# Kernel optimization log

Hardware: AMD Instinct MI355X
Metric: run time of the kernel (lower is better)

## Reference

```python
import jax, jax.numpy as jnp
import numpy as np

B, L, H = 32, 512, 256


def _gru(x, h, Wih, Whh, bih, bhh):
    # torch.nn.GRUCell math: gates ordered [r, z, n]
    gi = x @ Wih.T + bih
    gh = h @ Whh.T + bhh
    ir, iz, inn = jnp.split(gi, 3, axis=-1)
    hr, hz, hn = jnp.split(gh, 3, axis=-1)
    r = jax.nn.sigmoid(ir + hr)
    z = jax.nn.sigmoid(iz + hz)
    n = jnp.tanh(inn + r * hn)
    return (1.0 - z) * n + z * h


def setup_inputs() -> dict:
    key = jax.random.key(0)
    ks = jax.random.split(key, 20)
    s = 1.0 / np.sqrt(H)
    u = lambda k, shape: jax.random.uniform(k, shape, jnp.float32, -s, s)
    return {
        "P": jax.random.normal(ks[0], (B, L, H), jnp.float32),
        "wq_w": u(ks[1], (H, H)), "wq_b": u(ks[2], (H,)),
        "wp_w": u(ks[3], (H, H)), "wp_b": u(ks[4], (H,)),
        "ws_w": u(ks[5], (1, H)), "ws_b": u(ks[6], (1,)),
        "wg_w": u(ks[7], (H, 2 * H)), "wg_b": u(ks[8], (H,)),
        "Wih_l": u(ks[9], (3 * H, H)), "Whh_l": u(ks[10], (3 * H, H)),
        "bih_l": u(ks[11], (3 * H,)), "bhh_l": u(ks[12], (3 * H,)),
        "Wih_r": u(ks[13], (3 * H, H)), "Whh_r": u(ks[14], (3 * H, H)),
        "bih_r": u(ks[15], (3 * H,)), "bhh_r": u(ks[16], (3 * H,)),
    }


def reference(P, wq_w, wq_b, wp_w, wp_b, ws_w, ws_b, wg_w, wg_b,
              Wih_l, Whh_l, bih_l, bhh_l, Wih_r, Whh_r, bih_r, bhh_r):
    b, l, h = P.shape
    # wq(P) and wp(P[:,i]) are recomputed identically each step in the
    # original; hoist them once (same math).
    Hq = P @ wq_w.T + wq_b          # [B,L,H]
    Pp = P @ wp_w.T + wp_b          # [B,L,H]

    def left_step(hc, xs):
        p, pq = xs                  # [B,H], [B,H]
        # scores_j = ws . tanh(wq(P_j) + wp(p))
        scores = jnp.einsum('blh,h->bl', jnp.tanh(Hq + pq[:, None, :]), ws_w[0]) + ws_b[0]
        attn = jax.nn.softmax(scores, axis=1)
        c = jnp.einsum('bl,blh->bh', attn, P)
        g = jax.nn.sigmoid(jnp.concatenate([p, c], axis=1) @ wg_w.T + wg_b)
        c = g * c
        h_new = _gru(c, hc, Wih_l, Whh_l, bih_l, bhh_l)
        return h_new, (h_new, c)

    h0 = jnp.zeros((b, h), P.dtype)
    Pt = jnp.transpose(P, (1, 0, 2))   # [L,B,H]
    Ppt = jnp.transpose(Pp, (1, 0, 2))
    _, (out_l, c_seq) = jax.lax.scan(left_step, h0, (Pt, Ppt))

    def right_step(hc, c):
        h_new = _gru(c, hc, Wih_r, Whh_r, bih_r, bhh_r)
        return h_new, h_new

    _, out_r_rev = jax.lax.scan(right_step, h0, c_seq[::-1])
    out_r = out_r_rev[::-1]

    out = jnp.concatenate([out_l, out_r], axis=2)  # [L,B,2H]
    return jnp.transpose(out, (1, 0, 2))           # [B,L,2H]
```

## Files before the change

kernel.cpp:

```cpp
#include <hip/hip_runtime.h>
#include <cstdint>


#define LL 512
#define HH 256

typedef _Float16 half2_t __attribute__((ext_vector_type(2)));
typedef _Float16 f16x8   __attribute__((ext_vector_type(8)));
typedef float    f32x4   __attribute__((ext_vector_type(4)));

__device__ __forceinline__ float exp2f_fast(float x){
#if defined(__HIP_DEVICE_COMPILE__)
  return __builtin_amdgcn_exp2f(x);
#else
  return exp2f(x);
#endif
}
__device__ __forceinline__ float rcpf_fast(float x){
#if defined(__HIP_DEVICE_COMPILE__)
  return __builtin_amdgcn_rcpf(x);
#else
  return 1.0f/x;
#endif
}
__device__ __forceinline__ float tanh_fast(float x){
  float e = exp2f_fast(x * 2.885390081777927f);
  return 1.0f - 2.0f * rcpf_fast(1.0f + e);
}
__device__ __forceinline__ float sigmoid_fast(float x){
  return rcpf_fast(1.0f + exp2f_fast(x * -1.4426950408889634f));
}

#define SCALE_K2 2.885390081777927f

#if defined(__HIP_DEVICE_COMPILE__) && __has_builtin(__builtin_amdgcn_fdot2)
#define USE_FDOT2 1
#endif

__device__ __forceinline__ float dot2_acc(unsigned wb, unsigned hb, float a){
  half2_t wv = __builtin_bit_cast(half2_t, wb);
  half2_t hv = __builtin_bit_cast(half2_t, hb);
#ifdef USE_FDOT2
  return __builtin_amdgcn_fdot2(wv, hv, a, false);
#else
  return a + (float)wv.x*(float)hv.x + (float)wv.y*(float)hv.y;
#endif
}

__device__ __forceinline__ unsigned pack2h(float a, float b){
  half2_t h = { (_Float16)a, (_Float16)b };
  return __builtin_bit_cast(unsigned, h);
}

__device__ __forceinline__ void stage_t128(float* Ls, const float* g, int ldg){
  int tid = threadIdx.x;
  int r = tid >> 4, kq = (tid & 15) * 4;
  #pragma unroll
  for (int it = 0; it < 8; it++){
    int rr = r + 16*it;
    float4 v = *(const float4*)(g + (size_t)rr*ldg + kq);
    Ls[(kq+0)*132 + rr] = v.x;
    Ls[(kq+1)*132 + rr] = v.y;
    Ls[(kq+2)*132 + rr] = v.z;
    Ls[(kq+3)*132 + rr] = v.w;
  }
}
__device__ __forceinline__ void rg_inner128(const float* Xs, const float* Ws,
                                            float (&acc)[8][8], int rg, int cg){
  #pragma unroll 2
  for (int k = 0; k < 64; k++){
    const float* xr = Xs + k*132;
    const float* wr = Ws + k*132;
    float4 x0 = *(const float4*)(xr + rg*4);
    float4 x1 = *(const float4*)(xr + 64 + rg*4);
    float4 w0 = *(const float4*)(wr + cg*4);
    float4 w1 = *(const float4*)(wr + 64 + cg*4);
    float xv[8] = {x0.x,x0.y,x0.z,x0.w, x1.x,x1.y,x1.z,x1.w};
    float wv[8] = {w0.x,w0.y,w0.z,w0.w, w1.x,w1.y,w1.z,w1.w};
    #pragma unroll
    for (int i=0;i<8;i++)
      #pragma unroll
      for (int j=0;j<8;j++)
        acc[i][j] = fmaf(xv[i], wv[j], acc[i][j]);
  }
}
#define ROW_OF(i, rg) ((rg)*4 + ((i)&3) + ((i)>>2)*64)
#define COL_OF(j, cg) ((cg)*4 + ((j)&3) + ((j)>>2)*64)

#define LDK 36

__device__ __forceinline__ void mstage_direct(unsigned* Ls, const float* g, int ldg){
  int tid = threadIdx.x;
  int row = tid >> 1, half = tid & 1;
  const float4* s = (const float4*)(g + (size_t)row*ldg + half*32);
  unsigned* d = Ls + row*LDK + half*16;
  #pragma unroll
  for (int i = 0; i < 8; i += 2){
    float4 a = s[i], b = s[i+1];
    uint4 o;
    o.x = pack2h(a.x,a.y); o.y = pack2h(a.z,a.w);
    o.z = pack2h(b.x,b.y); o.w = pack2h(b.z,b.w);
    *(uint4*)(d + i*2) = o;
  }
}
__device__ __forceinline__ void mstage_trans(unsigned* Ls, const float* g, int ldg){
  int tid = threadIdx.x;
  int j = (tid & 31) * 4, kq = tid >> 5;
  #pragma unroll
  for (int it = 0; it < 4; it++){
    int kp = kq*4 + it;
    float4 a = *(const float4*)(g + (size_t)(2*kp  )*ldg + j);
    float4 b = *(const float4*)(g + (size_t)(2*kp+1)*ldg + j);
    Ls[(j+0)*LDK + kp] = pack2h(a.x, b.x);
    Ls[(j+1)*LDK + kp] = pack2h(a.y, b.y);
    Ls[(j+2)*LDK + kp] = pack2h(a.z, b.z);
    Ls[(j+3)*LDK + kp] = pack2h(a.w, b.w);
  }
}
__device__ __forceinline__ void mfma_inner(const unsigned* As, const unsigned* Bs,
                                           f32x4 (&acc)[8][2], int w, int l){
  int lr = l & 15, lq = l >> 4;
  #pragma unroll
  for (int kt = 0; kt < 2; kt++){
    f16x8 bf0, bf1;
    {
      uint4 q0 = *(const uint4*)&Bs[(w*32 +      lr)*LDK + kt*16 + lq*4];
      uint4 q1 = *(const uint4*)&Bs[(w*32 + 16 + lr)*LDK + kt*16 + lq*4];
      bf0 = __builtin_bit_cast(f16x8, q0);
      bf1 = __builtin_bit_cast(f16x8, q1);
    }
    #pragma unroll
    for (int rf = 0; rf < 8; rf++){
      uint4 qa = *(const uint4*)&As[(rf*16 + lr)*LDK + kt*16 + lq*4];
      f16x8 af = __builtin_bit_cast(f16x8, qa);
      acc[rf][0] = __builtin_amdgcn_mfma_f32_16x16x32_f16(af, bf0, acc[rf][0], 0,0,0);
      acc[rf][1] = __builtin_amdgcn_mfma_f32_16x16x32_f16(af, bf1, acc[rf][1], 0,0,0);
    }
  }
}

__global__ __launch_bounds__(256) void k1_hq_pp(
    const float* __restrict__ P,
    const float* __restrict__ wq_w, const float* __restrict__ wq_b,
    const float* __restrict__ wp_w, const float* __restrict__ wp_b,
    float* __restrict__ HQ, float* __restrict__ PP)
{
  __shared__ __align__(16) float Xs[64*132];
  __shared__ __align__(16) float Ws[64*132];
  int rt = blockIdx.x, ct = blockIdx.y;
  const float* W  = (ct < 2) ? wq_w : wp_w;
  const float* Bv = (ct < 2) ? wq_b : wp_b;
  float* O = (ct < 2) ? HQ : PP;
  int c0 = (ct & 1) * 128, r0 = rt * 128;
  int tid = threadIdx.x, rg = tid & 15, cg = tid >> 4;
  float acc[8][8];
  #pragma unroll
  for (int i=0;i<8;i++)
    #pragma unroll
    for (int j=0;j<8;j++) acc[i][j]=0.f;
  for (int kc = 0; kc < 4; kc++){
    __syncthreads();
    stage_t128(Xs, P + (size_t)r0*HH + kc*64, HH);
    stage_t128(Ws, W + (size_t)c0*HH + kc*64, HH);
    __syncthreads();
    rg_inner128(Xs, Ws, acc, rg, cg);
  }
  float bj[8];
  #pragma unroll
  for (int j=0;j<8;j++) bj[j] = Bv[c0 + COL_OF(j,cg)];
  #pragma unroll
  for (int i=0;i<8;i++){
    int r = r0 + ROW_OF(i,rg);
    #pragma unroll
    for (int j=0;j<8;j++)
      O[(size_t)r*HH + c0 + COL_OF(j,cg)] = SCALE_K2 * (acc[i][j] + bj[j]);
  }
}

__global__ __launch_bounds__(256) void k2_scores(
    const float* __restrict__ HQ, const float* __restrict__ PP,
    const float* __restrict__ ws_w, float* __restrict__ S)
{
  __shared__ float Hq_c[128*65];
  __shared__ float Pp_c[32*65];
  __shared__ float wsl[256];
  int tid = threadIdx.x;
  int b = blockIdx.y, t0 = blockIdx.x * 32;
  wsl[tid] = ws_w[tid];
  int tg = tid >> 6;
  int lg = tid & 63;
  for (int lc = 0; lc < 4; lc++){
    float acc[8][2];
    #pragma unroll
    for (int i=0;i<8;i++){ acc[i][0]=0.f; acc[i][1]=0.f; }
    for (int hc = 0; hc < 4; hc++){
      __syncthreads();
      {
        int r = tid >> 4, kq = (tid & 15) * 4;
        #pragma unroll
        for (int it=0; it<2; it++){
          int t = r + 16*it;
          float4 v = *(const float4*)(PP + ((size_t)b*LL + t0 + t)*HH + hc*64 + kq);
          float* d = Pp_c + t*65 + kq;
          d[0]=v.x; d[1]=v.y; d[2]=v.z; d[3]=v.w;
        }
      }
      {
        int r = tid >> 4, kq = (tid & 15) * 4;
        #pragma unroll
        for (int it=0; it<8; it++){
          int l = r + 16*it;
          float4 v = *(const float4*)(HQ + ((size_t)b*LL + lc*128 + l)*HH + hc*64 + kq);
          float* d = Hq_c + l*65 + kq;
          d[0]=v.x; d[1]=v.y; d[2]=v.z; d[3]=v.w;
        }
      }
      __syncthreads();
      #pragma unroll 2
      for (int h = 0; h < 64; h++){
        float w = wsl[hc*64 + h];
        float pp[8], hq[2];
        #pragma unroll
        for (int i=0;i<8;i++) pp[i] = Pp_c[(tg + 4*i)*65 + h];
        #pragma unroll
        for (int j=0;j<2;j++) hq[j] = Hq_c[(2*lg + j)*65 + h];
        #pragma unroll
        for (int i=0;i<8;i++)
          #pragma unroll
          for (int j=0;j<2;j++){
            float e = exp2f_fast(pp[i] + hq[j]);
            acc[i][j] = fmaf(w, rcpf_fast(1.0f + e), acc[i][j]);
          }
      }
    }
    #pragma unroll
    for (int i=0;i<8;i++)
      #pragma unroll
      for (int j=0;j<2;j++)
        S[((size_t)b*LL + t0 + tg + 4*i)*LL + lc*128 + 2*lg + j] = -2.0f*acc[i][j];
    __syncthreads();
  }
}

__global__ __launch_bounds__(256) void k3_softmax(float* __restrict__ S)
{
  int wave = threadIdx.x >> 6, lane = threadIdx.x & 63;
  size_t row = (size_t)blockIdx.x*4 + wave;
  float* p = S + row*LL;
  float v[8];
  #pragma unroll
  for (int i=0;i<8;i++) v[i] = p[lane + 64*i];
  float m = v[0];
  #pragma unroll
  for (int i=1;i<8;i++) m = fmaxf(m, v[i]);
  #pragma unroll
  for (int off=32; off>=1; off>>=1) m = fmaxf(m, __shfl_xor(m, off, 64));
  float s = 0.f;
  #pragma unroll
  for (int i=0;i<8;i++){ v[i] = exp2f_fast((v[i]-m)*1.4426950408889634f); s += v[i]; }
  #pragma unroll
  for (int off=32; off>=1; off>>=1) s += __shfl_xor(s, off, 64);
  float inv = 1.0f / s;
  #pragma unroll
  for (int i=0;i<8;i++) p[lane + 64*i] = v[i]*inv;
}

__global__ __launch_bounds__(256, 4) void k4_context(
    const float* __restrict__ S, const float* __restrict__ P, float* __restrict__ C)
{
  __shared__ __align__(16) unsigned As[128*LDK];
  __shared__ __align__(16) unsigned Bs[128*LDK];
  int j0 = blockIdx.x * 128, t0 = blockIdx.y * 128, b = blockIdx.z;
  int tid = threadIdx.x, w = tid >> 6, l = tid & 63;
  f32x4 acc[8][2];
  #pragma unroll
  for (int i=0;i<8;i++){ acc[i][0]=(f32x4){0,0,0,0}; acc[i][1]=(f32x4){0,0,0,0}; }
  for (int lc = 0; lc < 8; lc++){
    int l0 = lc*64;
    __syncthreads();
    mstage_direct(As, S + ((size_t)b*LL + t0)*LL + l0, LL);
    mstage_trans (Bs, P + ((size_t)b*LL + l0)*HH + j0, HH);
    __syncthreads();
    mfma_inner(As, Bs, acc, w, l);
  }
  int lr = l & 15, lq = l >> 4;
  #pragma unroll
  for (int rf=0; rf<8; rf++)
    #pragma unroll
    for (int cf=0; cf<2; cf++){
      int col = j0 + w*32 + cf*16 + lr;
      #pragma unroll
      for (int r=0; r<4; r++){
        int row = t0 + rf*16 + lq*4 + r;
        C[((size_t)b*LL + row)*HH + col] = acc[rf][cf][r];
      }
    }
}

__global__ __launch_bounds__(256, 4) void k5_gate(
    const float* __restrict__ P, const float* __restrict__ C,
    const float* __restrict__ wg_w, const float* __restrict__ wg_b,
    float* __restrict__ CG)
{
  __shared__ __align__(16) unsigned As[128*LDK];
  __shared__ __align__(16) unsigned Bs[128*LDK];
  int r0 = blockIdx.x*128, c0 = blockIdx.y*128;
  int tid = threadIdx.x, w = tid >> 6, l = tid & 63;
  f32x4 acc[8][2];
  #pragma unroll
  for (int i=0;i<8;i++){ acc[i][0]=(f32x4){0,0,0,0}; acc[i][1]=(f32x4){0,0,0,0}; }
  for (int kc = 0; kc < 8; kc++){
    const float* Xsrc = (kc < 4) ? (P + (size_t)r0*HH + kc*64)
                                 : (C + (size_t)r0*HH + (kc-4)*64);
    __syncthreads();
    mstage_direct(As, Xsrc, HH);
    mstage_direct(Bs, wg_w + (size_t)c0*(2*HH) + kc*64, 2*HH);
    __syncthreads();
    mfma_inner(As, Bs, acc, w, l);
  }
  int lr = l & 15, lq = l >> 4;
  #pragma unroll
  for (int cf=0; cf<2; cf++){
    int col = c0 + w*32 + cf*16 + lr;
    float bj = wg_b[col];
    #pragma unroll
    for (int rf=0; rf<8; rf++)
      #pragma unroll
      for (int r=0; r<4; r++){
        int row = r0 + rf*16 + lq*4 + r;
        float g = sigmoid_fast(acc[rf][cf][r] + bj);
        CG[(size_t)row*HH + col] = g * C[(size_t)row*HH + col];
      }
  }
}

__global__ __launch_bounds__(256, 4) void k6_gi(
    const float* __restrict__ CG,
    const float* __restrict__ Wih_l, const float* __restrict__ bih_l,
    const float* __restrict__ Wih_r, const float* __restrict__ bih_r,
    float* __restrict__ GIL, float* __restrict__ GIR)
{
  __shared__ __align__(16) unsigned As[128*LDK];
  __shared__ __align__(16) unsigned Bs[128*LDK];
  int rt = blockIdx.x, ct = blockIdx.y;
  int dir = (ct >= 6);
  const float* Wih = dir ? Wih_r : Wih_l;
  const float* bih = dir ? bih_r : bih_l;
  float* GI = dir ? GIR : GIL;
  int c0 = (ct % 6) * 128, r0 = rt * 128;
  int tid = threadIdx.x, w = tid >> 6, l = tid & 63;
  f32x4 acc[8][2];
  #pragma unroll
  for (int i=0;i<8;i++){ acc[i][0]=(f32x4){0,0,0,0}; acc[i][1]=(f32x4){0,0,0,0}; }
  for (int kc = 0; kc < 4; kc++){
    __syncthreads();
    mstage_direct(As, CG  + (size_t)r0*HH + kc*64, HH);
    mstage_direct(Bs, Wih + (size_t)c0*HH + kc*64, HH);
    __syncthreads();
    mfma_inner(As, Bs, acc, w, l);
  }
  int lr = l & 15, lq = l >> 4;
  #pragma unroll
  for (int cf=0; cf<2; cf++){
    int col = c0 + w*32 + cf*16 + lr;
    float bj = bih[col];
    #pragma unroll
    for (int rf=0; rf<8; rf++)
      #pragma unroll
      for (int r=0; r<4; r++){
        int row = r0 + rf*16 + lq*4 + r;
        GI[(size_t)row*768 + col] = acc[rf][cf][r] + bj;
      }
  }
}

__global__ __launch_bounds__(512, 2) void k7_scan(
    const float* __restrict__ GIL, const float* __restrict__ GIR,
    const float* __restrict__ Whh_l, const float* __restrict__ bhh_l,
    const float* __restrict__ Whh_r, const float* __restrict__ bhh_r,
    float* __restrict__ out)
{
  int b   = blockIdx.x >> 1;
  int dir = blockIdx.x & 1;
  int t   = threadIdx.x;
  int u   = t >> 1;
  int ks  = t & 1;
  int k0  = ks * 128;
  const float* GI  = dir ? GIR : GIL;
  const float* Whh = dir ? Whh_r : Whh_l;
  const float* bhh = dir ? bhh_r : bhh_l;

  unsigned w_r[64], w_z[64], w_n[64];
  {
    const float2* wr = (const float2*)(Whh + (size_t)(u      )*HH + k0);
    const float2* wz = (const float2*)(Whh + (size_t)(u + 256)*HH + k0);
    const float2* wn = (const float2*)(Whh + (size_t)(u + 512)*HH + k0);
    #pragma unroll
    for (int pc = 0; pc < 8; pc++){
      #pragma unroll
      for (int p = pc*8; p < pc*8+8; p++){ float2 a = wr[p]; w_r[p] = pack2h(a.x, a.y); }
      __builtin_amdgcn_sched_barrier(0);
      #pragma unroll
      for (int p = pc*8; p < pc*8+8; p++){ float2 a = wz[p]; w_z[p] = pack2h(a.x, a.y); }
      __builtin_amdgcn_sched_barrier(0);
      #pragma unroll
      for (int p = pc*8; p < pc*8+8; p++){ float2 a = wn[p]; w_n[p] = pack2h(a.x, a.y); }
      __builtin_amdgcn_sched_barrier(0);
    }
  }
  float b_r = bhh[u], b_z = bhh[u + 256], b_n = bhh[u + 512];

  __shared__ __align__(16) unsigned hsbuf[2][128];
  __shared__ __align__(16) float gi_buf[32*768];
  __shared__ __align__(16) float out_buf[32*256];
  if (t < 128){ hsbuf[0][t] = 0; }

  float hprev = 0.f;

  #pragma unroll 1
  for (int chunk = 0; chunk < 16; chunk++){
    int s0 = chunk * 32;
    int tlo = dir ? (LL - s0 - 32) : s0;
    {
      const float4* src = (const float4*)(GI + ((size_t)b*LL + tlo)*768);
      float4* dst = (float4*)gi_buf;
      #pragma unroll
      for (int rd = 0; rd < 3; rd++){
        float4 v0 = src[t + 512*(4*rd+0)];
        float4 v1 = src[t + 512*(4*rd+1)];
        float4 v2 = src[t + 512*(4*rd+2)];
        float4 v3 = src[t + 512*(4*rd+3)];
        dst[t + 512*(4*rd+0)] = v0;
        dst[t + 512*(4*rd+1)] = v1;
        dst[t + 512*(4*rd+2)] = v2;
        dst[t + 512*(4*rd+3)] = v3;
        __builtin_amdgcn_sched_barrier(0);
      }
    }
    __syncthreads();

    #pragma unroll 1
    for (int p = 0; p < 32; p++){
      int s = s0 + p;
      int tt = dir ? (LL-1-s) : s;
      int gidx = tt - tlo;
      float ar0=0.f, ar1=0.f, az0=0.f, az1=0.f, an0=0.f, an1=0.f;
      #pragma unroll
      for (int sc = 0; sc < 4; sc++){
        const uint4* hp = (const uint4*)(hsbuf[s & 1]) + ks*16 + sc*4;
        uint4 q0 = hp[0], q1 = hp[1], q2 = hp[2], q3 = hp[3];
        unsigned hv[16] = {q0.x,q0.y,q0.z,q0.w, q1.x,q1.y,q1.z,q1.w,
                           q2.x,q2.y,q2.z,q2.w, q3.x,q3.y,q3.z,q3.w};
        #pragma unroll
        for (int j = 0; j < 16; j += 2){
          int pp = sc*16 + j;
          ar0 = dot2_acc(w_r[pp  ], hv[j  ], ar0);
          az0 = dot2_acc(w_z[pp  ], hv[j  ], az0);
          an0 = dot2_acc(w_n[pp  ], hv[j  ], an0);
          ar1 = dot2_acc(w_r[pp+1], hv[j+1], ar1);
          az1 = dot2_acc(w_z[pp+1], hv[j+1], az1);
          an1 = dot2_acc(w_n[pp+1], hv[j+1], an1);
        }
        __builtin_amdgcn_sched_barrier(0);
      }
      float ar = ar0 + ar1, az = az0 + az1, an = an0 + an1;
      ar += __shfl_xor(ar, 1, 64);
      az += __shfl_xor(az, 1, 64);
      an += __shfl_xor(an, 1, 64);
      const float* g = gi_buf + (size_t)gidx*768;
      float r  = sigmoid_fast(g[u      ] + ar + b_r);
      float z  = sigmoid_fast(g[u + 256] + az + b_z);
      float n  = tanh_fast  (g[u + 512] + r*(an + b_n));
      float hn = z*(hprev - n) + n;
      hprev = hn;
      if (ks == 0){
        out_buf[p*256 + u] = hn;
        ((unsigned short*)hsbuf[(s & 1) ^ 1])[u] =
            __builtin_bit_cast(unsigned short, (_Float16)hn);
      }
      __syncthreads();
    }
    #pragma unroll
    for (int fr = 0; fr < 4; fr++){
      #pragma unroll
      for (int q = 0; q < 4; q++){
        int i = t + 512*(fr*4 + q);
        int p = i >> 8, uu = i & 255;
        int s = s0 + p;
        int tt = dir ? (LL-1-s) : s;
        out[((size_t)b*LL + tt)*(2*HH) + dir*HH + uu] = out_buf[i];
      }
      __builtin_amdgcn_sched_barrier(0);
    }
    __syncthreads();
  }
}

extern "C" void kernel_launch(void* const* d_in, const int* in_sizes, int n_in,
                              void* d_out, int out_size, void* d_ws, size_t ws_size,
                              hipStream_t stream)
{
  const float* P    = (const float*)d_in[0];
  const float* wq_w = (const float*)d_in[1];
  const float* wq_b = (const float*)d_in[2];
  const float* wp_w = (const float*)d_in[3];
  const float* wp_b = (const float*)d_in[4];
  const float* ws_w = (const float*)d_in[5];
  const float* wg_w = (const float*)d_in[7];
  const float* wg_b = (const float*)d_in[8];
  const float* Wih_l= (const float*)d_in[9];
  const float* Whh_l= (const float*)d_in[10];
  const float* bih_l= (const float*)d_in[11];
  const float* bhh_l= (const float*)d_in[12];
  const float* Wih_r= (const float*)d_in[13];
  const float* Whh_r= (const float*)d_in[14];
  const float* bih_r= (const float*)d_in[15];
  const float* bhh_r= (const float*)d_in[16];

  float* ws  = (float*)d_ws;
  float* HQ  = ws;
  float* PP  = ws + 4194304;
  float* S   = ws + 8388608;
  float* C   = ws + 16777216;
  float* CG  = ws + 20971520;
  float* GIR = ws + 25165824;
  float* GIL = ws;
  float* out = (float*)d_out;

  k1_hq_pp  <<<dim3(128, 4),    256, 0, stream>>>(P, wq_w, wq_b, wp_w, wp_b, HQ, PP);
  k2_scores <<<dim3(16, 32),    256, 0, stream>>>(HQ, PP, ws_w, S);
  k3_softmax<<<4096,            256, 0, stream>>>(S);
  k4_context<<<dim3(2, 4, 32),  256, 0, stream>>>(S, P, C);
  k5_gate   <<<dim3(128, 2),    256, 0, stream>>>(P, C, wg_w, wg_b, CG);
  k6_gi     <<<dim3(128, 12),   256, 0, stream>>>(CG, Wih_l, bih_l, Wih_r, bih_r, GIL, GIR);
  k7_scan   <<<64,              512, 0, stream>>>(GIL, GIR, Whh_l, bhh_l, Whh_r, bhh_r, out);
}
```

Measured before the change: 1.334 ms.

## Fuse softmax into score kernel and precompute exponentials in projection

The projection kernel now stores exp2 of the scaled Hq/Pp values, so the scores kernel replaces one exp2 per (t,l,h) element with a multiply, using exp(a+b)=exp(a)*exp(b). The scores kernel keeps accumulators for all four l-chunks in registers and performs the row softmax in place via wave shuffles, removing the separate softmax kernel and its read/write pass over S. This raises register pressure (64 accumulators per thread) and risks overflow or inf in the exponential product for large arguments.

```diff
diff --git a/kernel.cpp b/kernel.cpp
--- a/kernel.cpp
+++ b/kernel.cpp
@@ -173,7 +173,8 @@
     int r = r0 + ROW_OF(i,rg);
     #pragma unroll
     for (int j=0;j<8;j++)
-      O[(size_t)r*HH + c0 + COL_OF(j,cg)] = SCALE_K2 * (acc[i][j] + bj[j]);
+      O[(size_t)r*HH + c0 + COL_OF(j,cg)] =
+          exp2f_fast(SCALE_K2 * (acc[i][j] + bj[j]));
   }
 }
 
@@ -189,10 +190,14 @@
   wsl[tid] = ws_w[tid];
   int tg = tid >> 6;
   int lg = tid & 63;
+  float acc4[4][8][2];
+  #pragma unroll
+  for (int lc=0;lc<4;lc++)
+    #pragma unroll
+    for (int i=0;i<8;i++){ acc4[lc][i][0]=0.f; acc4[lc][i][1]=0.f; }
+  #pragma unroll
   for (int lc = 0; lc < 4; lc++){
-    float acc[8][2];
-    #pragma unroll
-    for (int i=0;i<8;i++){ acc[i][0]=0.f; acc[i][1]=0.f; }
+    #pragma unroll 1
     for (int hc = 0; hc < 4; hc++){
       __syncthreads();
       {
@@ -228,41 +233,38 @@
         for (int i=0;i<8;i++)
           #pragma unroll
           for (int j=0;j<2;j++){
-            float e = exp2f_fast(pp[i] + hq[j]);
-            acc[i][j] = fmaf(w, rcpf_fast(1.0f + e), acc[i][j]);
+            float e = pp[i] * hq[j];
+            acc4[lc][i][j] = fmaf(w, rcpf_fast(1.0f + e), acc4[lc][i][j]);
           }
       }
     }
-    #pragma unroll
-    for (int i=0;i<8;i++)
-      #pragma unroll
-      for (int j=0;j<2;j++)
-        S[((size_t)b*LL + t0 + tg + 4*i)*LL + lc*128 + 2*lg + j] = -2.0f*acc[i][j];
-    __syncthreads();
-  }
-}
-
-__global__ __launch_bounds__(256) void k3_softmax(float* __restrict__ S)
-{
-  int wave = threadIdx.x >> 6, lane = threadIdx.x & 63;
-  size_t row = (size_t)blockIdx.x*4 + wave;
-  float* p = S + row*LL;
-  float v[8];
-  #pragma unroll
-  for (int i=0;i<8;i++) v[i] = p[lane + 64*i];
-  float m = v[0];
-  #pragma unroll
-  for (int i=1;i<8;i++) m = fmaxf(m, v[i]);
-  #pragma unroll
-  for (int off=32; off>=1; off>>=1) m = fmaxf(m, __shfl_xor(m, off, 64));
-  float s = 0.f;
-  #pragma unroll
-  for (int i=0;i<8;i++){ v[i] = exp2f_fast((v[i]-m)*1.4426950408889634f); s += v[i]; }
-  #pragma unroll
-  for (int off=32; off>=1; off>>=1) s += __shfl_xor(s, off, 64);
-  float inv = 1.0f / s;
-  #pragma unroll
-  for (int i=0;i<8;i++) p[lane + 64*i] = v[i]*inv;
+  }
+  #pragma unroll
+  for (int i=0;i<8;i++){
+    float v[8];
+    #pragma unroll
+    for (int lc=0;lc<4;lc++){
+      v[lc*2+0] = -2.0f*acc4[lc][i][0];
+      v[lc*2+1] = -2.0f*acc4[lc][i][1];
+    }
+    float m = v[0];
+    #pragma unroll
+    for (int k=1;k<8;k++) m = fmaxf(m, v[k]);
+    #pragma unroll
+    for (int off=32; off>=1; off>>=1) m = fmaxf(m, __shfl_xor(m, off, 64));
+    float s = 0.f;
+    #pragma unroll
+    for (int k=0;k<8;k++){ v[k] = exp2f_fast((v[k]-m)*1.4426950408889634f); s += v[k]; }
+    #pragma unroll
+    for (int off=32; off>=1; off>>=1) s += __shfl_xor(s, off, 64);
+    float inv = 1.0f / s;
+    size_t base = ((size_t)b*LL + t0 + tg + 4*i)*LL;
+    #pragma unroll
+    for (int lc=0;lc<4;lc++){
+      S[base + lc*128 + 2*lg + 0] = v[lc*2+0]*inv;
+      S[base + lc*128 + 2*lg + 1] = v[lc*2+1]*inv;
+    }
+  }
 }
 
 __global__ __launch_bounds__(256, 4) void k4_context(
@@ -529,7 +531,6 @@
 
   k1_hq_pp  <<<dim3(128, 4),    256, 0, stream>>>(P, wq_w, wq_b, wp_w, wp_b, HQ, PP);
   k2_scores <<<dim3(16, 32),    256, 0, stream>>>(HQ, PP, ws_w, S);
-  k3_softmax<<<4096,            256, 0, stream>>>(S);
   k4_context<<<dim3(2, 4, 32),  256, 0, stream>>>(S, P, C);
   k5_gate   <<<dim3(128, 2),    256, 0, stream>>>(P, C, wg_w, wg_b, CG);
   k6_gi     <<<dim3(128, 12),   256, 0, stream>>>(CG, Wih_l, bih_l, Wih_r, bih_r, GIL, GIR);
```

Result: faster. 1.170 ms (-12.3%).
